# Kernel tuning notes

Hardware: AMD Instinct MI355X
Metric: run time of the kernel (lower is better)

The kernel has to match this reference:

```python
import jax, jax.numpy as jnp
import numpy as np

N, E, L, HID, HEADS, G = 50000, 800000, 2, 128, 8, 256
DK = HID // HEADS

def _ln(x, g, b, eps=1e-5):
    m = jnp.mean(x, axis=-1, keepdims=True)
    v = jnp.mean((x - m) ** 2, axis=-1, keepdims=True)
    return (x - m) * jax.lax.rsqrt(v + eps) * g + b

def setup_inputs() -> dict:
    key = jax.random.key(0)
    ks = jax.random.split(key, 24)
    rn = lambda i, s: (0.05 * jax.random.normal(ks[i], s)).astype(jnp.float32)
    return {
        'node_attr': jax.random.randint(ks[0], (N, 4), 0, 64, dtype=jnp.int32),
        'batch_idx': jnp.sort(jax.random.randint(ks[1], (N,), 0, G, dtype=jnp.int32)),
        'edge_index': jax.random.randint(ks[2], (2, E), 0, N, dtype=jnp.int32),
        'strat_dist': jax.random.randint(ks[3], (E,), 0, 32, dtype=jnp.int32),
        'strat_path': jax.random.randint(ks[4], (E,), 0, 16, dtype=jnp.int32),
        'atom_emb': rn(5, (4, 64, HID)),
        'dist_emb': rn(6, (L, 32, HID)),
        'path_emb': rn(7, (L, 16, HID)),
        'Wq': rn(8, (L, HID, HID)), 'bq': rn(9, (L, HID)),
        'Wk': rn(10, (L, HID, HID)), 'bk': rn(11, (L, HID)),
        'Wv': rn(12, (L, HID, HID)), 'bv': rn(13, (L, HID)),
        'Wa': rn(14, (L, HID, HID)), 'ba': rn(15, (L, HID)),
        'ln1_g': jnp.ones((L, HID), jnp.float32), 'ln1_b': jnp.zeros((L, HID), jnp.float32),
        'Wmid': rn(16, (L, HID, 2 * HID)), 'bmid': rn(17, (L, 2 * HID)),
        'Wo': rn(18, (L, 2 * HID, HID)), 'bo': rn(19, (L, HID)),
        'ln2_g': jnp.ones((L, HID), jnp.float32), 'ln2_b': jnp.zeros((L, HID), jnp.float32),
        'W_out': rn(20, (HID, 1)), 'b_out': jnp.zeros((1,), jnp.float32),
    }

def reference(node_attr, batch_idx, edge_index, strat_dist, strat_path,
              atom_emb, dist_emb, path_emb, Wq, bq, Wk, bk, Wv, bv, Wa, ba,
              ln1_g, ln1_b, Wmid, bmid, Wo, bo, ln2_g, ln2_b, W_out, b_out):
    # node encoder: sum of per-feature embeddings (AtomEncoder style)
    x = sum(atom_emb[f][node_attr[:, f]] for f in range(node_attr.shape[1]))  # [N, HID]
    src, tgt = edge_index[0], edge_index[1]  # j (source), i (target)
    inv_sqrt_dk = np.float32(1.0 / np.sqrt(DK))
    for l in range(L):
        # per-edge gather + relational encodings added to the source vector
        s = x[src] + dist_emb[l][strat_dist] + path_emb[l][strat_path]  # [E, HID]
        t = x[tgt]                                                      # [E, HID]
        q = (t @ Wq[l] + bq[l]).reshape(E, HEADS, DK)
        k = (s @ Wk[l] + bk[l]).reshape(E, HEADS, DK)
        v = (s @ Wv[l] + bv[l]).reshape(E, HEADS, DK)
        scores = jnp.sum(q * k, axis=-1) * inv_sqrt_dk  # [E, HEADS]
        # segment softmax keyed on target node id
        smax = jax.ops.segment_max(scores, tgt, num_segments=N)
        ex = jnp.exp(scores - smax[tgt])
        den = jax.ops.segment_sum(ex, tgt, num_segments=N)
        att = ex / (den[tgt] + 1e-16)                   # [E, HEADS]
        msg = (v * att[:, :, None]).reshape(E, HID)
        aggr = jax.ops.segment_sum(msg, tgt, num_segments=N)  # scatter-add
        # update: attn FFN + residual + LayerNorms (dropout is identity in eval)
        h = _ln(jax.nn.gelu(aggr, approximate=False) @ Wa[l] + ba[l] + x, ln1_g[l], ln1_b[l])
        h2 = jax.nn.gelu(h @ Wmid[l] + bmid[l], approximate=False) @ Wo[l] + bo[l]
        x = _ln(h2 + h, ln2_g[l], ln2_b[l])
    # global mean pool per graph, then readout
    cnt = jax.ops.segment_sum(jnp.ones((N,), x.dtype), batch_idx, num_segments=G)
    pooled = jax.ops.segment_sum(x, batch_idx, num_segments=G) / jnp.maximum(cnt, 1.0)[:, None]
    return pooled @ W_out + b_out
```

## Files before the change

### kernel.cpp

```cpp
#include <hip/hip_runtime.h>
#include <hip/hip_bf16.h>
#include <math.h>
#include <stdint.h>

#define N_NODES 50000
#define N_EDGES 800000
#define HID 128
#define NGRAPH 256
#define NLAYER 2
#define CAP 64

typedef __bf16 bf16x8 __attribute__((ext_vector_type(8)));
typedef __bf16 bf16x2 __attribute__((ext_vector_type(2)));
typedef float f32x4 __attribute__((ext_vector_type(4)));
typedef float f32x2 __attribute__((ext_vector_type(2)));

__device__ __forceinline__ float gelu_f(float v) {
    return 0.5f * v * (1.0f + erff(v * 0.70710678118654752f));
}

__device__ __forceinline__ void cvt4_fp8(uint32_t w, float* o) {
    f32x2 lo = __builtin_amdgcn_cvt_pk_f32_fp8(w, false);
    f32x2 hi = __builtin_amdgcn_cvt_pk_f32_fp8(w, true);
    o[0] = lo[0]; o[1] = lo[1]; o[2] = hi[0]; o[3] = hi[1];
}
__device__ __forceinline__ uint32_t pk4_fp8(float a, float b, float c, float d) {
    int w = __builtin_amdgcn_cvt_pk_fp8_f32(a, b, 0, false);
    w = __builtin_amdgcn_cvt_pk_fp8_f32(c, d, w, true);
    return (uint32_t)w;
}

__global__ __launch_bounds__(256) void prep_kernel(
    const int* __restrict__ tgt, const int* __restrict__ src,
    const int* __restrict__ sd, const int* __restrict__ sp,
    int* __restrict__ cnt, uint32_t* __restrict__ ei,
    const int* __restrict__ attr, const float* __restrict__ aemb,
    float* __restrict__ x, __bf16* __restrict__ xb,
    const float* __restrict__ de, const float* __restrict__ pe,
    const float* __restrict__ Wk, const float* __restrict__ Wv,
    __bf16* __restrict__ tkv,
    const float* __restrict__ Wq, const float* __restrict__ Wa,
    const float* __restrict__ Wmid, const float* __restrict__ Wo,
    __bf16* __restrict__ wqkvf, __bf16* __restrict__ waf,
    __bf16* __restrict__ wmidf, __bf16* __restrict__ wof,
    const int* __restrict__ batch, const float* __restrict__ bout,
    const float* __restrict__ bq, const float* __restrict__ bk,
    const float* __restrict__ bv,
    float* __restrict__ invc, float* __restrict__ outp, float* __restrict__ bqkv) {
    __shared__ float sde[128];
    int b = blockIdx.x;
    int tid = threadIdx.x;
    if (b < 3125) {
        int e = b * 256 + tid;
        int t = tgt[e];
        int r = atomicAdd(&cnt[t], 1);
        if (r < CAP) ei[(t << 6) + r] = (uint32_t)src[e] | ((uint32_t)((sd[e] << 4) | sp[e]) << 16);
    } else if (b < 28125) {
        int idx = (b - 3125) * 256 + tid;
        int n = idx >> 7, c = idx & 127;
        const int4 a = *(const int4*)(attr + n * 4);
        float s = aemb[(0 * 64 + a.x) * 128 + c] + aemb[(1 * 64 + a.y) * 128 + c] +
                  aemb[(2 * 64 + a.z) * 128 + c] + aemb[(3 * 64 + a.w) * 128 + c];
        x[idx] = s;
        xb[idx] = (__bf16)s;
    } else if (b < 29149) {
        int bb = b - 28125;
        int l = bb >> 9;
        int md = bb & 511;
        int dd = md >> 4, pp = md & 15;
        int c = tid;
        if (c < 128) sde[c] = de[l * 4096 + dd * 128 + c] + pe[l * 2048 + pp * 128 + c];
        __syncthreads();
        const float* W = (c < 128) ? (Wk + l * 16384) : (Wv + l * 16384);
        int cc = c & 127;
        float acc = 0.f;
#pragma unroll 4
        for (int k = 0; k < 128; k++) acc = fmaf(sde[k], W[k * 128 + cc], acc);
        tkv[(size_t)bb * 256 + c] = (__bf16)acc;
    } else if (b < 29277) {
        int u = (b - 29149) * 256 + tid;
        int l = u >> 14, r = u & 16383;
        const float* srcp;
        __bf16* dstp;
        int kg, scol, srcCO;
        if (r < 6144) {
            kg = r / 384;
            int uu = r % 384;
            int sec = uu >> 7, cc = uu & 127;
            scol = ((cc & 15) << 3) | (cc >> 4);
            const float* Ws = (sec == 0) ? Wq : (sec == 1) ? Wk : Wv;
            srcp = Ws + l * 16384;
            srcCO = 128;
            dstp = wqkvf + (size_t)l * 49152 + (size_t)r * 8;
        } else if (r < 8192) {
            int rr = r - 6144;
            kg = rr >> 7;
            int cc = rr & 127;
            scol = ((cc & 15) << 3) | (cc >> 4);
            srcp = Wa + l * 16384;
            srcCO = 128;
            dstp = waf + (size_t)l * 16384 + (size_t)rr * 8;
        } else if (r < 12288) {
            int rr = r - 8192;
            kg = rr >> 8;
            int uu = rr & 255;
            int blk = uu >> 7, cc = uu & 127;
            scol = blk * 128 + (((cc & 15) << 3) | (cc >> 4));
            srcp = Wmid + l * 32768;
            srcCO = 256;
            dstp = wmidf + (size_t)l * 32768 + (size_t)rr * 8;
        } else {
            int rr = r - 12288;
            kg = rr >> 7;
            int cc = rr & 127;
            scol = ((cc & 15) << 3) | (cc >> 4);
            srcp = Wo + l * 32768;
            srcCO = 128;
            dstp = wof + (size_t)l * 32768 + (size_t)rr * 8;
        }
        bf16x8 o;
#pragma unroll
        for (int j = 0; j < 8; j++) o[j] = (__bf16)srcp[(kg * 8 + j) * srcCO + scol];
        *(bf16x8*)dstp = o;
    } else {
        int sb = b - 29277;
        if (sb == 0) {
            int g = tid;
            int lo = 0, hi = N_NODES;
            while (lo < hi) { int mid = (lo + hi) >> 1; if (batch[mid] < g) lo = mid + 1; else hi = mid; }
            int start = lo;
            lo = start; hi = N_NODES;
            while (lo < hi) { int mid = (lo + hi) >> 1; if (batch[mid] < g + 1) lo = mid + 1; else hi = mid; }
            int c2 = lo - start;
            invc[g] = 1.0f / fmaxf((float)c2, 1.0f);
            outp[g] = bout[0];
        } else {
            int r = (sb - 1) * 256 + tid;
            int l = r / 384, c = r % 384;
            float v = (c < 128) ? bq[l * 128 + c]
                    : (c < 256) ? bk[l * 128 + c - 128]
                                : bv[l * 128 + c - 256];
            bqkv[r] = v;
        }
    }
}

__global__ __launch_bounds__(256) void qkv_gemm(
    const __bf16* __restrict__ A, const __bf16* __restrict__ Wf,
    const float* __restrict__ bias, __bf16* __restrict__ Qb,
    uint8_t* __restrict__ kv8, int M) {
    int lane = threadIdx.x & 63;
    int wv = threadIdx.x >> 6;
    int row0 = blockIdx.y * 64 + wv * 16;
    int sec = blockIdx.x;
    int col0 = sec * 128;
    if (row0 >= M) return;
    int quad = lane >> 4, tq = lane & 15;
    f32x4 acc[8] = {};
#pragma unroll
    for (int k0 = 0; k0 < 128; k0 += 32) {
        int rr = row0 + tq;
        if (rr >= M) rr = M - 1;
        bf16x8 af = *(const bf16x8*)(A + (size_t)rr * 128 + k0 + quad * 8);
#pragma unroll
        for (int nt = 0; nt < 8; nt++) {
            bf16x8 bfr = *(const bf16x8*)(Wf + ((size_t)((k0 >> 3) + quad) * 384 + col0 + nt * 16 + tq) * 8);
            acc[nt] = __builtin_amdgcn_mfma_f32_16x16x32_bf16(af, bfr, acc[nt], 0, 0, 0);
        }
    }
    int cb = tq * 8;
    float bia[8];
#pragma unroll
    for (int t = 0; t < 8; t++) bia[t] = bias[col0 + cb + t];
#pragma unroll
    for (int v = 0; v < 4; v++) {
        int rr = row0 + quad * 4 + v;
        if (rr >= M) continue;
        float val[8];
#pragma unroll
        for (int t = 0; t < 8; t++) val[t] = acc[t][v] + bia[t];
        if (sec == 0) {
            bf16x8 ov;
#pragma unroll
            for (int t = 0; t < 8; t++) ov[t] = (__bf16)val[t];
            *(bf16x8*)(Qb + (size_t)rr * 128 + cb) = ov;
        } else {
            uint2 st;
            st.x = pk4_fp8(val[0], val[1], val[2], val[3]);
            st.y = pk4_fp8(val[4], val[5], val[6], val[7]);
            *(uint2*)(kv8 + (size_t)rr * 256 + (sec - 1) * 128 + cb) = st;
        }
    }
}

template <int CI, bool GOUT, bool LN, bool POOL>
__global__ __launch_bounds__(256) void mfma_gemm(
    const __bf16* __restrict__ A, const __bf16* __restrict__ Wf,
    const float* __restrict__ bias, const float* __restrict__ res,
    const float* __restrict__ lng, const float* __restrict__ lnb,
    float* outf, __bf16* outb,
    const int* __restrict__ batch, const float* __restrict__ invc,
    const float* __restrict__ WoutV, float* __restrict__ outp,
    int M, int CO) {
    __shared__ float ps[POOL ? NGRAPH : 1];
    int lane = threadIdx.x & 63;
    int wv = threadIdx.x >> 6;
    int row0 = blockIdx.y * 64 + wv * 16;
    int col0 = blockIdx.x * 128;
    bool active = row0 < M;
    if (POOL) {
        ps[threadIdx.x] = 0.f;
        __syncthreads();
    } else if (!active) {
        return;
    }
    int quad = lane >> 4, tq = lane & 15;
    if (active) {
        f32x4 acc[8] = {};
#pragma unroll
        for (int k0 = 0; k0 < CI; k0 += 32) {
            int rr = row0 + tq;
            if (rr >= M) rr = M - 1;
            bf16x8 af = *(const bf16x8*)(A + (size_t)rr * CI + k0 + quad * 8);
#pragma unroll
            for (int nt = 0; nt < 8; nt++) {
                bf16x8 bfr = *(const bf16x8*)(Wf + ((size_t)((k0 >> 3) + quad) * CO + col0 + nt * 16 + tq) * 8);
                acc[nt] = __builtin_amdgcn_mfma_f32_16x16x32_bf16(af, bfr, acc[nt], 0, 0, 0);
            }
        }
        int cb = col0 + tq * 8;
        float bia[8] = {};
        if (bias) {
#pragma unroll
            for (int t = 0; t < 8; t++) bia[t] = bias[cb + t];
        }
        float gv[8], bv2[8];
        if (LN) {
#pragma unroll
            for (int t = 0; t < 8; t++) { gv[t] = lng[cb + t]; bv2[t] = lnb[cb + t]; }
        }
        float wo8[8];
        if (POOL) {
#pragma unroll
            for (int t = 0; t < 8; t++) wo8[t] = WoutV[cb + t];
        }
#pragma unroll
        for (int v = 0; v < 4; v++) {
            int rr = row0 + quad * 4 + v;
            if (rr >= M) continue;
            float val[8];
#pragma unroll
            for (int nt = 0; nt < 8; nt++) val[nt] = acc[nt][v] + bia[nt];
            if (res) {
                float4 r0 = *(const float4*)(res + (size_t)rr * 128 + tq * 8);
                float4 r1 = *(const float4*)(res + (size_t)rr * 128 + tq * 8 + 4);
                val[0] += r0.x; val[1] += r0.y; val[2] += r0.z; val[3] += r0.w;
                val[4] += r1.x; val[5] += r1.y; val[6] += r1.z; val[7] += r1.w;
            }
            if (GOUT) {
#pragma unroll
                for (int t = 0; t < 8; t++) val[t] = gelu_f(val[t]);
            }
            if (LN) {
                float s = 0.f, s2 = 0.f;
#pragma unroll
                for (int t = 0; t < 8; t++) { s += val[t]; s2 = fmaf(val[t], val[t], s2); }
#pragma unroll
                for (int o = 1; o < 16; o <<= 1) {
                    s += __shfl_xor(s, o);
                    s2 += __shfl_xor(s2, o);
                }
                float m = s * (1.0f / 128.0f);
                float var = s2 * (1.0f / 128.0f) - m * m;
                float rs = rsqrtf(var + 1e-5f);
#pragma unroll
                for (int t = 0; t < 8; t++) val[t] = (val[t] - m) * rs * gv[t] + bv2[t];
            }
            if (outf) {
                *(float4*)(outf + (size_t)rr * CO + cb) = make_float4(val[0], val[1], val[2], val[3]);
                *(float4*)(outf + (size_t)rr * CO + cb + 4) = make_float4(val[4], val[5], val[6], val[7]);
            }
            if (outb) {
                bf16x8 ov;
#pragma unroll
                for (int t = 0; t < 8; t++) ov[t] = (__bf16)val[t];
                *(bf16x8*)(outb + (size_t)rr * CO + cb) = ov;
            }
            if (POOL) {
                float dot = 0.f;
#pragma unroll
                for (int t = 0; t < 8; t++) dot = fmaf(val[t], wo8[t], dot);
#pragma unroll
                for (int o = 1; o < 16; o <<= 1) dot += __shfl_xor(dot, o);
                if (tq == 0) {
                    int g = batch[rr];
                    atomicAdd(&ps[g], dot * invc[g]);
                }
            }
        }
    }
    if (POOL) {
        __syncthreads();
        float pv = ps[threadIdx.x];
        if (pv != 0.f) atomicAdd(&outp[threadIdx.x], pv);
    }
}

__global__ __launch_bounds__(256) void attn_kernel(
    const __bf16* __restrict__ Qb, const uint8_t* __restrict__ kv8,
    const __bf16* __restrict__ tkv,
    const int* __restrict__ cnt, const uint32_t* __restrict__ ei,
    __bf16* __restrict__ outb) {
    __shared__ float red[4][1376];
    int wv = threadIdx.x >> 6;
    int i = blockIdx.x * 4 + wv;
    int lane = threadIdx.x & 63;
    int slot = lane >> 3, h = lane & 7;
    int ch0 = h * 16;
    const __bf16* qp = Qb + (size_t)i * 128 + ch0;
    bf16x8 q0 = *(const bf16x8*)qp;
    bf16x8 q1 = *(const bf16x8*)(qp + 8);
    float qf[16];
#pragma unroll
    for (int t = 0; t < 8; t++) { qf[t] = (float)q0[t]; qf[8 + t] = (float)q1[t]; }
    int deg = cnt[i];
    if (deg > CAP) deg = CAP;
    int p0 = i << 6;
    int p1 = p0 + deg;
    float l = 0.f;
    float a[16] = {};
    int p = p0 + slot;
    uint32_t w1 = 0, w2 = 0;
    if (p < p1) w1 = ei[p];
    if (p + 8 < p1) w2 = ei[p + 8];
    uint4 kw, vw;
    bf16x8 t0, t1, u0, u1;
    {
        int j = w1 & 0xffff, md = w1 >> 16;
        const uint8_t* kr = kv8 + (size_t)j * 256 + ch0;
        kw = *(const uint4*)kr;
        vw = *(const uint4*)(kr + 128);
        const __bf16* tr = tkv + md * 256 + ch0;
        t0 = *(const bf16x8*)tr;
        t1 = *(const bf16x8*)(tr + 8);
        u0 = *(const bf16x8*)(tr + 128);
        u1 = *(const bf16x8*)(tr + 136);
    }
    while (p < p1) {
        uint4 kwn, vwn;
        bf16x8 t0n, t1n, u0n, u1n;
        {
            int j = w2 & 0xffff, md = w2 >> 16;
            const uint8_t* kr = kv8 + (size_t)j * 256 + ch0;
            kwn = *(const uint4*)kr;
            vwn = *(const uint4*)(kr + 128);
            const __bf16* tr = tkv + md * 256 + ch0;
            t0n = *(const bf16x8*)tr;
            t1n = *(const bf16x8*)(tr + 8);
            u0n = *(const bf16x8*)(tr + 128);
            u1n = *(const bf16x8*)(tr + 136);
        }
        uint32_t w3 = w2;
        if (p + 16 < p1) w3 = ei[p + 16];
        float kf[16], vf[16];
        cvt4_fp8(kw.x, kf + 0); cvt4_fp8(kw.y, kf + 4);
        cvt4_fp8(kw.z, kf + 8); cvt4_fp8(kw.w, kf + 12);
        cvt4_fp8(vw.x, vf + 0); cvt4_fp8(vw.y, vf + 4);
        cvt4_fp8(vw.z, vf + 8); cvt4_fp8(vw.w, vf + 12);
        float s = 0.f;
#pragma unroll
        for (int t = 0; t < 8; t++) {
            s = fmaf(qf[t], kf[t] + (float)t0[t], s);
            s = fmaf(qf[8 + t], kf[8 + t] + (float)t1[t], s);
        }
        float pe = __expf(s * 0.25f);
        l += pe;
#pragma unroll
        for (int t = 0; t < 8; t++) {
            a[t] = fmaf(pe, vf[t] + (float)u0[t], a[t]);
            a[8 + t] = fmaf(pe, vf[8 + t] + (float)u1[t], a[8 + t]);
        }
        kw = kwn; vw = vwn; t0 = t0n; t1 = t1n; u0 = u0n; u1 = u1n;
        w2 = w3;
        p += 8;
    }
    float* rw = red[wv] + slot * 172 + 20 * h;
    *(float4*)(rw + 0) = make_float4(a[0], a[1], a[2], a[3]);
    *(float4*)(rw + 4) = make_float4(a[4], a[5], a[6], a[7]);
    *(float4*)(rw + 8) = make_float4(a[8], a[9], a[10], a[11]);
    *(float4*)(rw + 12) = make_float4(a[12], a[13], a[14], a[15]);
    red[wv][slot * 172 + 156 + h] = l;
    asm volatile("" ::: "memory");
    int pc = 2 * lane + 4 * (lane >> 3);
    int hh = lane >> 3;
    float s0 = 0.f, s1 = 0.f, ls = 0.f;
#pragma unroll
    for (int s = 0; s < 8; s++) {
        float2 v = *(const float2*)(red[wv] + s * 172 + pc);
        s0 += v.x;
        s1 += v.y;
        ls += red[wv][s * 172 + 156 + hh];
    }
    float inv = 1.0f / (ls + 1e-16f);
    bf16x2 o2;
    o2[0] = (__bf16)gelu_f(s0 * inv);
    o2[1] = (__bf16)gelu_f(s1 * inv);
    *(bf16x2*)(outb + (size_t)i * 128 + 2 * lane) = o2;
}

extern "C" void kernel_launch(void* const* d_in, const int* in_sizes, int n_in,
                              void* d_out, int out_size, void* d_ws, size_t ws_size,
                              hipStream_t stream) {
    const int N = N_NODES, E = N_EDGES;
    const int* node_attr = (const int*)d_in[0];
    const int* batch_idx = (const int*)d_in[1];
    const int* edge_index = (const int*)d_in[2];
    const int* strat_dist = (const int*)d_in[3];
    const int* strat_path = (const int*)d_in[4];
    const float* atom_emb = (const float*)d_in[5];
    const float* dist_emb = (const float*)d_in[6];
    const float* path_emb = (const float*)d_in[7];
    const float* Wq = (const float*)d_in[8];
    const float* bq = (const float*)d_in[9];
    const float* Wk = (const float*)d_in[10];
    const float* bk = (const float*)d_in[11];
    const float* Wv = (const float*)d_in[12];
    const float* bv = (const float*)d_in[13];
    const float* Wa = (const float*)d_in[14];
    const float* ba = (const float*)d_in[15];
    const float* ln1g = (const float*)d_in[16];
    const float* ln1b = (const float*)d_in[17];
    const float* Wmid = (const float*)d_in[18];
    const float* bmid = (const float*)d_in[19];
    const float* Wo = (const float*)d_in[20];
    const float* bo = (const float*)d_in[21];
    const float* ln2g = (const float*)d_in[22];
    const float* ln2b = (const float*)d_in[23];
    const float* Wout = (const float*)d_in[24];
    const float* bout = (const float*)d_in[25];
    float* out = (float*)d_out;

    const int* src = edge_index;
    const int* tgt = edge_index + E;

    size_t NF = (size_t)N * HID;
    float* x = (float*)d_ws;
    float* invc = x + NF;
    float* bqkv = invc + 256;
    __bf16* xb = (__bf16*)(bqkv + 768);
    __bf16* Qb = xb + NF;
    __bf16* ab = Qb + NF;
    __bf16* midb = ab + NF;
    __bf16* tkv = midb + 2 * NF;
    __bf16* wqkvf = tkv + 262144;
    __bf16* waf = wqkvf + 98304;
    __bf16* wmidf = waf + 32768;
    __bf16* wof = wmidf + 65536;
    uint8_t* kv8 = (uint8_t*)(wof + 65536);
    uint32_t* ei = (uint32_t*)(kv8 + (size_t)N * 256);
    int* cnt = (int*)(ei + (size_t)N * CAP);

    hipMemsetAsync(cnt, 0, N * sizeof(int), stream);
    prep_kernel<<<29281, 256, 0, stream>>>(
        tgt, src, strat_dist, strat_path, cnt, ei,
        node_attr, atom_emb, x, xb,
        dist_emb, path_emb, Wk, Wv, tkv,
        Wq, Wa, Wmid, Wo, wqkvf, waf, wmidf, wof,
        batch_idx, bout, bq, bk, bv, invc, out, bqkv);

    const int GB = (N + 63) / 64;
    const int AB = (N + 3) / 4;

    for (int l = 0; l < NLAYER; ++l) {
        qkv_gemm<<<dim3(3, GB), 256, 0, stream>>>(
            xb, wqkvf + l * 49152, bqkv + l * 384, Qb, kv8, N);

        attn_kernel<<<AB, 256, 0, stream>>>(Qb, kv8, tkv + l * 131072, cnt, ei, ab);

        mfma_gemm<128, false, true, false><<<dim3(1, GB), 256, 0, stream>>>(
            ab, waf + l * 16384, ba + l * 128, x, ln1g + l * 128, ln1b + l * 128,
            x, ab, nullptr, nullptr, nullptr, nullptr, N, 128);
        mfma_gemm<128, true, false, false><<<dim3(2, GB), 256, 0, stream>>>(
            ab, wmidf + l * 32768, bmid + l * 256, nullptr, nullptr, nullptr,
            nullptr, midb, nullptr, nullptr, nullptr, nullptr, N, 256);
        if (l < NLAYER - 1) {
            mfma_gemm<256, false, true, false><<<dim3(1, GB), 256, 0, stream>>>(
                midb, wof + l * 32768, bo + l * 128, x, ln2g + l * 128, ln2b + l * 128,
                x, xb, nullptr, nullptr, nullptr, nullptr, N, 128);
        } else {
            mfma_gemm<256, false, true, true><<<dim3(1, GB), 256, 0, stream>>>(
                midb, wof + l * 32768, bo + l * 128, x, ln2g + l * 128, ln2b + l * 128,
                nullptr, nullptr, batch_idx, invc, Wout, out, N, 128);
        }
    }
}
```

Measured before the change: 450.5 us.

## Drop fp32 residual stream, keep bf16 residuals, and double GEMM row tile

Removes the fp32 copy of the node state x and uses the bf16 activations (xb and ab) as residual inputs to the LayerNorm GEMMs. This cuts fp32 residual reads and writes in each layer. Separately, each wave now computes 32 rows instead of 16, so every weight fragment load is reused across two MFMAs, and the grid is halved. The cost is lower residual precision, which could affect accuracy, plus more accumulator registers and fewer blocks.

```diff
diff --git a/kernel.cpp b/kernel.cpp
--- a/kernel.cpp
+++ b/kernel.cpp
@@ -35,7 +35,7 @@
     const int* __restrict__ sd, const int* __restrict__ sp,
     int* __restrict__ cnt, uint32_t* __restrict__ ei,
     const int* __restrict__ attr, const float* __restrict__ aemb,
-    float* __restrict__ x, __bf16* __restrict__ xb,
+    __bf16* __restrict__ xb,
     const float* __restrict__ de, const float* __restrict__ pe,
     const float* __restrict__ Wk, const float* __restrict__ Wv,
     __bf16* __restrict__ tkv,
@@ -61,7 +61,6 @@
         const int4 a = *(const int4*)(attr + n * 4);
         float s = aemb[(0 * 64 + a.x) * 128 + c] + aemb[(1 * 64 + a.y) * 128 + c] +
                   aemb[(2 * 64 + a.z) * 128 + c] + aemb[(3 * 64 + a.w) * 128 + c];
-        x[idx] = s;
         xb[idx] = (__bf16)s;
     } else if (b < 29149) {
         int bb = b - 28125;
@@ -151,21 +150,26 @@
     uint8_t* __restrict__ kv8, int M) {
     int lane = threadIdx.x & 63;
     int wv = threadIdx.x >> 6;
-    int row0 = blockIdx.y * 64 + wv * 16;
+    int row0 = blockIdx.y * 128 + wv * 32;
     int sec = blockIdx.x;
     int col0 = sec * 128;
     if (row0 >= M) return;
     int quad = lane >> 4, tq = lane & 15;
-    f32x4 acc[8] = {};
+    f32x4 acc[2][8] = {};
 #pragma unroll
     for (int k0 = 0; k0 < 128; k0 += 32) {
-        int rr = row0 + tq;
-        if (rr >= M) rr = M - 1;
-        bf16x8 af = *(const bf16x8*)(A + (size_t)rr * 128 + k0 + quad * 8);
+        bf16x8 af[2];
+#pragma unroll
+        for (int mt = 0; mt < 2; mt++) {
+            int rr = row0 + mt * 16 + tq;
+            if (rr >= M) rr = M - 1;
+            af[mt] = *(const bf16x8*)(A + (size_t)rr * 128 + k0 + quad * 8);
+        }
 #pragma unroll
         for (int nt = 0; nt < 8; nt++) {
             bf16x8 bfr = *(const bf16x8*)(Wf + ((size_t)((k0 >> 3) + quad) * 384 + col0 + nt * 16 + tq) * 8);
-            acc[nt] = __builtin_amdgcn_mfma_f32_16x16x32_bf16(af, bfr, acc[nt], 0, 0, 0);
+            acc[0][nt] = __builtin_amdgcn_mfma_f32_16x16x32_bf16(af[0], bfr, acc[0][nt], 0, 0, 0);
+            acc[1][nt] = __builtin_amdgcn_mfma_f32_16x16x32_bf16(af[1], bfr, acc[1][nt], 0, 0, 0);
         }
     }
     int cb = tq * 8;
@@ -173,22 +177,25 @@
 #pragma unroll
     for (int t = 0; t < 8; t++) bia[t] = bias[col0 + cb + t];
 #pragma unroll
-    for (int v = 0; v < 4; v++) {
-        int rr = row0 + quad * 4 + v;
-        if (rr >= M) continue;
-        float val[8];
-#pragma unroll
-        for (int t = 0; t < 8; t++) val[t] = acc[t][v] + bia[t];
-        if (sec == 0) {
-            bf16x8 ov;
-#pragma unroll
-            for (int t = 0; t < 8; t++) ov[t] = (__bf16)val[t];
-            *(bf16x8*)(Qb + (size_t)rr * 128 + cb) = ov;
-        } else {
-            uint2 st;
-            st.x = pk4_fp8(val[0], val[1], val[2], val[3]);
-            st.y = pk4_fp8(val[4], val[5], val[6], val[7]);
-            *(uint2*)(kv8 + (size_t)rr * 256 + (sec - 1) * 128 + cb) = st;
+    for (int mt = 0; mt < 2; mt++) {
+#pragma unroll
+        for (int v = 0; v < 4; v++) {
+            int rr = row0 + mt * 16 + quad * 4 + v;
+            if (rr >= M) continue;
+            float val[8];
+#pragma unroll
+            for (int t = 0; t < 8; t++) val[t] = acc[mt][t][v] + bia[t];
+            if (sec == 0) {
+                bf16x8 ov;
+#pragma unroll
+                for (int t = 0; t < 8; t++) ov[t] = (__bf16)val[t];
+                *(bf16x8*)(Qb + (size_t)rr * 128 + cb) = ov;
+            } else {
+                uint2 st;
+                st.x = pk4_fp8(val[0], val[1], val[2], val[3]);
+                st.y = pk4_fp8(val[4], val[5], val[6], val[7]);
+                *(uint2*)(kv8 + (size_t)rr * 256 + (sec - 1) * 128 + cb) = st;
+            }
         }
     }
 }
@@ -196,16 +203,16 @@
 template <int CI, bool GOUT, bool LN, bool POOL>
 __global__ __launch_bounds__(256) void mfma_gemm(
     const __bf16* __restrict__ A, const __bf16* __restrict__ Wf,
-    const float* __restrict__ bias, const float* __restrict__ res,
+    const float* __restrict__ bias, const __bf16* __restrict__ res,
     const float* __restrict__ lng, const float* __restrict__ lnb,
-    float* outf, __bf16* outb,
+    __bf16* outb,
     const int* __restrict__ batch, const float* __restrict__ invc,
     const float* __restrict__ WoutV, float* __restrict__ outp,
     int M, int CO) {
     __shared__ float ps[POOL ? NGRAPH : 1];
     int lane = threadIdx.x & 63;
     int wv = threadIdx.x >> 6;
-    int row0 = blockIdx.y * 64 + wv * 16;
+    int row0 = blockIdx.y * 128 + wv * 32;
     int col0 = blockIdx.x * 128;
     bool active = row0 < M;
     if (POOL) {
@@ -216,16 +223,21 @@
     }
     int quad = lane >> 4, tq = lane & 15;
     if (active) {
-        f32x4 acc[8] = {};
+        f32x4 acc[2][8] = {};
 #pragma unroll
         for (int k0 = 0; k0 < CI; k0 += 32) {
-            int rr = row0 + tq;
-            if (rr >= M) rr = M - 1;
-            bf16x8 af = *(const bf16x8*)(A + (size_t)rr * CI + k0 + quad * 8);
+            bf16x8 af[2];
+#pragma unroll
+            for (int mt = 0; mt < 2; mt++) {
+                int rr = row0 + mt * 16 + tq;
+                if (rr >= M) rr = M - 1;
+                af[mt] = *(const bf16x8*)(A + (size_t)rr * CI + k0 + quad * 8);
+            }
 #pragma unroll
             for (int nt = 0; nt < 8; nt++) {
                 bf16x8 bfr = *(const bf16x8*)(Wf + ((size_t)((k0 >> 3) + quad) * CO + col0 + nt * 16 + tq) * 8);
-                acc[nt] = __builtin_amdgcn_mfma_f32_16x16x32_bf16(af, bfr, acc[nt], 0, 0, 0);
+                acc[0][nt] = __builtin_amdgcn_mfma_f32_16x16x32_bf16(af[0], bfr, acc[0][nt], 0, 0, 0);
+                acc[1][nt] = __builtin_amdgcn_mfma_f32_16x16x32_bf16(af[1], bfr, acc[1][nt], 0, 0, 0);
             }
         }
         int cb = col0 + tq * 8;
@@ -245,56 +257,54 @@
             for (int t = 0; t < 8; t++) wo8[t] = WoutV[cb + t];
         }
 #pragma unroll
-        for (int v = 0; v < 4; v++) {
-            int rr = row0 + quad * 4 + v;
-            if (rr >= M) continue;
-            float val[8];
-#pragma unroll
-            for (int nt = 0; nt < 8; nt++) val[nt] = acc[nt][v] + bia[nt];
-            if (res) {
-                float4 r0 = *(const float4*)(res + (size_t)rr * 128 + tq * 8);
-                float4 r1 = *(const float4*)(res + (size_t)rr * 128 + tq * 8 + 4);
-                val[0] += r0.x; val[1] += r0.y; val[2] += r0.z; val[3] += r0.w;
-                val[4] += r1.x; val[5] += r1.y; val[6] += r1.z; val[7] += r1.w;
-            }
-            if (GOUT) {
-#pragma unroll
-                for (int t = 0; t < 8; t++) val[t] = gelu_f(val[t]);
-            }
-            if (LN) {
-                float s = 0.f, s2 = 0.f;
-#pragma unroll
-                for (int t = 0; t < 8; t++) { s += val[t]; s2 = fmaf(val[t], val[t], s2); }
-#pragma unroll
-                for (int o = 1; o < 16; o <<= 1) {
-                    s += __shfl_xor(s, o);
-                    s2 += __shfl_xor(s2, o);
+        for (int mt = 0; mt < 2; mt++) {
+#pragma unroll
+            for (int v = 0; v < 4; v++) {
+                int rr = row0 + mt * 16 + quad * 4 + v;
+                if (rr >= M) continue;
+                float val[8];
+#pragma unroll
+                for (int nt = 0; nt < 8; nt++) val[nt] = acc[mt][nt][v] + bia[nt];
+                if (res) {
+                    bf16x8 rv = *(const bf16x8*)(res + (size_t)rr * 128 + tq * 8);
+#pragma unroll
+                    for (int t = 0; t < 8; t++) val[t] += (float)rv[t];
                 }
-                float m = s * (1.0f / 128.0f);
-                float var = s2 * (1.0f / 128.0f) - m * m;
-                float rs = rsqrtf(var + 1e-5f);
-#pragma unroll
-                for (int t = 0; t < 8; t++) val[t] = (val[t] - m) * rs * gv[t] + bv2[t];
-            }
-            if (outf) {
-                *(float4*)(outf + (size_t)rr * CO + cb) = make_float4(val[0], val[1], val[2], val[3]);
-                *(float4*)(outf + (size_t)rr * CO + cb + 4) = make_float4(val[4], val[5], val[6], val[7]);
-            }
-            if (outb) {
-                bf16x8 ov;
-#pragma unroll
-                for (int t = 0; t < 8; t++) ov[t] = (__bf16)val[t];
-                *(bf16x8*)(outb + (size_t)rr * CO + cb) = ov;
-            }
-            if (POOL) {
-                float dot = 0.f;
-#pragma unroll
-                for (int t = 0; t < 8; t++) dot = fmaf(val[t], wo8[t], dot);
-#pragma unroll
-                for (int o = 1; o < 16; o <<= 1) dot += __shfl_xor(dot, o);
-                if (tq == 0) {
-                    int g = batch[rr];
-                    atomicAdd(&ps[g], dot * invc[g]);
+                if (GOUT) {
+#pragma unroll
+                    for (int t = 0; t < 8; t++) val[t] = gelu_f(val[t]);
+                }
+                if (LN) {
+                    float s = 0.f, s2 = 0.f;
+#pragma unroll
+                    for (int t = 0; t < 8; t++) { s += val[t]; s2 = fmaf(val[t], val[t], s2); }
+#pragma unroll
+                    for (int o = 1; o < 16; o <<= 1) {
+                        s += __shfl_xor(s, o);
+                        s2 += __shfl_xor(s2, o);
+                    }
+                    float m = s * (1.0f / 128.0f);
+                    float var = s2 * (1.0f / 128.0f) - m * m;
+                    float rs = rsqrtf(var + 1e-5f);
+#pragma unroll
+                    for (int t = 0; t < 8; t++) val[t] = (val[t] - m) * rs * gv[t] + bv2[t];
+                }
+                if (outb) {
+                    bf16x8 ov;
+#pragma unroll
+                    for (int t = 0; t < 8; t++) ov[t] = (__bf16)val[t];
+                    *(bf16x8*)(outb + (size_t)rr * CO + cb) = ov;
+                }
+                if (POOL) {
+                    float dot = 0.f;
+#pragma unroll
+                    for (int t = 0; t < 8; t++) dot = fmaf(val[t], wo8[t], dot);
+#pragma unroll
+                    for (int o = 1; o < 16; o <<= 1) dot += __shfl_xor(dot, o);
+                    if (tq == 0) {
+                        int g = batch[rr];
+                        atomicAdd(&ps[g], dot * invc[g]);
+                    }
                 }
             }
         }
@@ -444,8 +454,7 @@
     const int* tgt = edge_index + E;
 
     size_t NF = (size_t)N * HID;
-    float* x = (float*)d_ws;
-    float* invc = x + NF;
+    float* invc = (float*)d_ws;
     float* bqkv = invc + 256;
     __bf16* xb = (__bf16*)(bqkv + 768);
     __bf16* Qb = xb + NF;
@@ -463,12 +472,12 @@
     hipMemsetAsync(cnt, 0, N * sizeof(int), stream);
     prep_kernel<<<29281, 256, 0, stream>>>(
         tgt, src, strat_dist, strat_path, cnt, ei,
-        node_attr, atom_emb, x, xb,
+        node_attr, atom_emb, xb,
         dist_emb, path_emb, Wk, Wv, tkv,
         Wq, Wa, Wmid, Wo, wqkvf, waf, wmidf, wof,
         batch_idx, bout, bq, bk, bv, invc, out, bqkv);
 
-    const int GB = (N + 63) / 64;
+    const int GB = (N + 127) / 128;
     const int AB = (N + 3) / 4;
 
     for (int l = 0; l < NLAYER; ++l) {
@@ -478,19 +487,19 @@
         attn_kernel<<<AB, 256, 0, stream>>>(Qb, kv8, tkv + l * 131072, cnt, ei, ab);
 
         mfma_gemm<128, false, true, false><<<dim3(1, GB), 256, 0, stream>>>(
-            ab, waf + l * 16384, ba + l * 128, x, ln1g + l * 128, ln1b + l * 128,
-            x, ab, nullptr, nullptr, nullptr, nullptr, N, 128);
+            ab, waf + l * 16384, ba + l * 128, xb, ln1g + l * 128, ln1b + l * 128,
+            ab, nullptr, nullptr, nullptr, nullptr, N, 128);
         mfma_gemm<128, true, false, false><<<dim3(2, GB), 256, 0, stream>>>(
             ab, wmidf + l * 32768, bmid + l * 256, nullptr, nullptr, nullptr,
-            nullptr, midb, nullptr, nullptr, nullptr, nullptr, N, 256);
+            midb, nullptr, nullptr, nullptr, nullptr, N, 256);
         if (l < NLAYER - 1) {
             mfma_gemm<256, false, true, false><<<dim3(1, GB), 256, 0, stream>>>(
-                midb, wof + l * 32768, bo + l * 128, x, ln2g + l * 128, ln2b + l * 128,
-                x, xb, nullptr, nullptr, nullptr, nullptr, N, 128);
+                midb, wof + l * 32768, bo + l * 128, ab, ln2g + l * 128, ln2b + l * 128,
+                xb, nullptr, nullptr, nullptr, nullptr, N, 128);
         } else {
             mfma_gemm<256, false, true, true><<<dim3(1, GB), 256, 0, stream>>>(
-                midb, wof + l * 32768, bo + l * 128, x, ln2g + l * 128, ln2b + l * 128,
-                nullptr, nullptr, batch_idx, invc, Wout, out, N, 128);
-        }
-    }
-}
+                midb, wof + l * 32768, bo + l * 128, ab, ln2g + l * 128, ln2b + l * 128,
+                nullptr, batch_idx, invc, Wout, out, N, 128);
+        }
+    }
+}
```

New measurement: 466.4 us. 3.5% more time.

## Drop fp32 residual stream and fuse edge bucketing into first QKV GEMM

Applied to the files above, without the earlier changes.

Removes the fp32 copy of node features x. Residuals are now read from the bf16 buffers (xb, ab), which cuts global read/write traffic in the LN GEMMs and the prep kernel. Edge bucketing by target moves out of prep_kernel into extra blocks of the layer-0 qkv_gemm launch, so the atomic scatter overlaps with GEMM work. Each bucketing thread now handles two edges. The risk is lower residual precision (bf16 instead of fp32) and more accumulated error in the output.

```diff
diff --git a/kernel.cpp b/kernel.cpp
--- a/kernel.cpp
+++ b/kernel.cpp
@@ -31,11 +31,8 @@
 }
 
 __global__ __launch_bounds__(256) void prep_kernel(
-    const int* __restrict__ tgt, const int* __restrict__ src,
-    const int* __restrict__ sd, const int* __restrict__ sp,
-    int* __restrict__ cnt, uint32_t* __restrict__ ei,
     const int* __restrict__ attr, const float* __restrict__ aemb,
-    float* __restrict__ x, __bf16* __restrict__ xb,
+    __bf16* __restrict__ xb,
     const float* __restrict__ de, const float* __restrict__ pe,
     const float* __restrict__ Wk, const float* __restrict__ Wv,
     __bf16* __restrict__ tkv,
@@ -50,21 +47,15 @@
     __shared__ float sde[128];
     int b = blockIdx.x;
     int tid = threadIdx.x;
-    if (b < 3125) {
-        int e = b * 256 + tid;
-        int t = tgt[e];
-        int r = atomicAdd(&cnt[t], 1);
-        if (r < CAP) ei[(t << 6) + r] = (uint32_t)src[e] | ((uint32_t)((sd[e] << 4) | sp[e]) << 16);
-    } else if (b < 28125) {
-        int idx = (b - 3125) * 256 + tid;
+    if (b < 25000) {
+        int idx = b * 256 + tid;
         int n = idx >> 7, c = idx & 127;
         const int4 a = *(const int4*)(attr + n * 4);
         float s = aemb[(0 * 64 + a.x) * 128 + c] + aemb[(1 * 64 + a.y) * 128 + c] +
                   aemb[(2 * 64 + a.z) * 128 + c] + aemb[(3 * 64 + a.w) * 128 + c];
-        x[idx] = s;
         xb[idx] = (__bf16)s;
-    } else if (b < 29149) {
-        int bb = b - 28125;
+    } else if (b < 26024) {
+        int bb = b - 25000;
         int l = bb >> 9;
         int md = bb & 511;
         int dd = md >> 4, pp = md & 15;
@@ -77,8 +68,8 @@
 #pragma unroll 4
         for (int k = 0; k < 128; k++) acc = fmaf(sde[k], W[k * 128 + cc], acc);
         tkv[(size_t)bb * 256 + c] = (__bf16)acc;
-    } else if (b < 29277) {
-        int u = (b - 29149) * 256 + tid;
+    } else if (b < 26152) {
+        int u = (b - 26024) * 256 + tid;
         int l = u >> 14, r = u & 16383;
         const float* srcp;
         __bf16* dstp;
@@ -123,7 +114,7 @@
         for (int j = 0; j < 8; j++) o[j] = (__bf16)srcp[(kg * 8 + j) * srcCO + scol];
         *(bf16x8*)dstp = o;
     } else {
-        int sb = b - 29277;
+        int sb = b - 26152;
         if (sb == 0) {
             int g = tid;
             int lo = 0, hi = N_NODES;
@@ -145,14 +136,43 @@
     }
 }
 
+#define SCATB 1563
 __global__ __launch_bounds__(256) void qkv_gemm(
     const __bf16* __restrict__ A, const __bf16* __restrict__ Wf,
     const float* __restrict__ bias, __bf16* __restrict__ Qb,
-    uint8_t* __restrict__ kv8, int M) {
-    int lane = threadIdx.x & 63;
-    int wv = threadIdx.x >> 6;
-    int row0 = blockIdx.y * 64 + wv * 16;
-    int sec = blockIdx.x;
+    uint8_t* __restrict__ kv8, int M, int scatN,
+    const int* __restrict__ tgt, const int* __restrict__ src,
+    const int* __restrict__ sd, const int* __restrict__ sp,
+    int* __restrict__ cnt, uint32_t* __restrict__ ei) {
+    int tid = threadIdx.x;
+    if (blockIdx.x < (unsigned)scatN) {
+        int e0 = blockIdx.x * 512 + tid;
+        int e1 = e0 + 256;
+        bool v1 = e1 < N_EDGES;
+        bool v0 = e0 < N_EDGES;
+        int t0 = 0, t1 = 0;
+        uint32_t p0 = 0, p1 = 0;
+        if (v0) {
+            t0 = tgt[e0];
+            p0 = (uint32_t)src[e0] | ((uint32_t)((sd[e0] << 4) | sp[e0]) << 16);
+        }
+        if (v1) {
+            t1 = tgt[e1];
+            p1 = (uint32_t)src[e1] | ((uint32_t)((sd[e1] << 4) | sp[e1]) << 16);
+        }
+        int r0 = CAP, r1 = CAP;
+        if (v0) r0 = atomicAdd(&cnt[t0], 1);
+        if (v1) r1 = atomicAdd(&cnt[t1], 1);
+        if (v0 && r0 < CAP) ei[(t0 << 6) + r0] = p0;
+        if (v1 && r1 < CAP) ei[(t1 << 6) + r1] = p1;
+        return;
+    }
+    int bq = blockIdx.x - scatN;
+    int sec = bq % 3;
+    int rowblk = bq / 3;
+    int lane = tid & 63;
+    int wv = tid >> 6;
+    int row0 = rowblk * 64 + wv * 16;
     int col0 = sec * 128;
     if (row0 >= M) return;
     int quad = lane >> 4, tq = lane & 15;
@@ -196,9 +216,9 @@
 template <int CI, bool GOUT, bool LN, bool POOL>
 __global__ __launch_bounds__(256) void mfma_gemm(
     const __bf16* __restrict__ A, const __bf16* __restrict__ Wf,
-    const float* __restrict__ bias, const float* __restrict__ res,
+    const float* __restrict__ bias, const __bf16* __restrict__ res,
     const float* __restrict__ lng, const float* __restrict__ lnb,
-    float* outf, __bf16* outb,
+    __bf16* outb,
     const int* __restrict__ batch, const float* __restrict__ invc,
     const float* __restrict__ WoutV, float* __restrict__ outp,
     int M, int CO) {
@@ -252,10 +272,9 @@
 #pragma unroll
             for (int nt = 0; nt < 8; nt++) val[nt] = acc[nt][v] + bia[nt];
             if (res) {
-                float4 r0 = *(const float4*)(res + (size_t)rr * 128 + tq * 8);
-                float4 r1 = *(const float4*)(res + (size_t)rr * 128 + tq * 8 + 4);
-                val[0] += r0.x; val[1] += r0.y; val[2] += r0.z; val[3] += r0.w;
-                val[4] += r1.x; val[5] += r1.y; val[6] += r1.z; val[7] += r1.w;
+                bf16x8 rv = *(const bf16x8*)(res + (size_t)rr * 128 + tq * 8);
+#pragma unroll
+                for (int t = 0; t < 8; t++) val[t] += (float)rv[t];
             }
             if (GOUT) {
 #pragma unroll
@@ -275,10 +294,6 @@
                 float rs = rsqrtf(var + 1e-5f);
 #pragma unroll
                 for (int t = 0; t < 8; t++) val[t] = (val[t] - m) * rs * gv[t] + bv2[t];
-            }
-            if (outf) {
-                *(float4*)(outf + (size_t)rr * CO + cb) = make_float4(val[0], val[1], val[2], val[3]);
-                *(float4*)(outf + (size_t)rr * CO + cb + 4) = make_float4(val[4], val[5], val[6], val[7]);
             }
             if (outb) {
                 bf16x8 ov;
@@ -444,8 +459,7 @@
     const int* tgt = edge_index + E;
 
     size_t NF = (size_t)N * HID;
-    float* x = (float*)d_ws;
-    float* invc = x + NF;
+    float* invc = (float*)d_ws;
     float* bqkv = invc + 256;
     __bf16* xb = (__bf16*)(bqkv + 768);
     __bf16* Qb = xb + NF;
@@ -461,9 +475,8 @@
     int* cnt = (int*)(ei + (size_t)N * CAP);
 
     hipMemsetAsync(cnt, 0, N * sizeof(int), stream);
-    prep_kernel<<<29281, 256, 0, stream>>>(
-        tgt, src, strat_dist, strat_path, cnt, ei,
-        node_attr, atom_emb, x, xb,
+    prep_kernel<<<26156, 256, 0, stream>>>(
+        node_attr, atom_emb, xb,
         dist_emb, path_emb, Wk, Wv, tkv,
         Wq, Wa, Wmid, Wo, wqkvf, waf, wmidf, wof,
         batch_idx, bout, bq, bk, bv, invc, out, bqkv);
@@ -472,25 +485,27 @@
     const int AB = (N + 3) / 4;
 
     for (int l = 0; l < NLAYER; ++l) {
-        qkv_gemm<<<dim3(3, GB), 256, 0, stream>>>(
-            xb, wqkvf + l * 49152, bqkv + l * 384, Qb, kv8, N);
+        int scatN = (l == 0) ? SCATB : 0;
+        qkv_gemm<<<scatN + 3 * GB, 256, 0, stream>>>(
+            xb, wqkvf + l * 49152, bqkv + l * 384, Qb, kv8, N, scatN,
+            tgt, src, strat_dist, strat_path, cnt, ei);
 
         attn_kernel<<<AB, 256, 0, stream>>>(Qb, kv8, tkv + l * 131072, cnt, ei, ab);
 
         mfma_gemm<128, false, true, false><<<dim3(1, GB), 256, 0, stream>>>(
-            ab, waf + l * 16384, ba + l * 128, x, ln1g + l * 128, ln1b + l * 128,
-            x, ab, nullptr, nullptr, nullptr, nullptr, N, 128);
+            ab, waf + l * 16384, ba + l * 128, xb, ln1g + l * 128, ln1b + l * 128,
+            ab, nullptr, nullptr, nullptr, nullptr, N, 128);
         mfma_gemm<128, true, false, false><<<dim3(2, GB), 256, 0, stream>>>(
             ab, wmidf + l * 32768, bmid + l * 256, nullptr, nullptr, nullptr,
-            nullptr, midb, nullptr, nullptr, nullptr, nullptr, N, 256);
+            midb, nullptr, nullptr, nullptr, nullptr, N, 256);
         if (l < NLAYER - 1) {
             mfma_gemm<256, false, true, false><<<dim3(1, GB), 256, 0, stream>>>(
-                midb, wof + l * 32768, bo + l * 128, x, ln2g + l * 128, ln2b + l * 128,
-                x, xb, nullptr, nullptr, nullptr, nullptr, N, 128);
+                midb, wof + l * 32768, bo + l * 128, ab, ln2g + l * 128, ln2b + l * 128,
+                xb, nullptr, nullptr, nullptr, nullptr, N, 128);
         } else {
             mfma_gemm<256, false, true, true><<<dim3(1, GB), 256, 0, stream>>>(
-                midb, wof + l * 32768, bo + l * 128, x, ln2g + l * 128, ln2b + l * 128,
-                nullptr, nullptr, batch_idx, invc, Wout, out, N, 128);
-        }
-    }
-}
+                midb, wof + l * 32768, bo + l * 128, ab, ln2g + l * 128, ln2b + l * 128,
+                nullptr, batch_idx, invc, Wout, out, N, 128);
+        }
+    }
+}
```

Measured after the change: 429.4 us. 4.7% less time.
